# Optimization experiments

Hardware: AMD Instinct MI355X
Metric: run time of the kernel (lower is better)

Reference implementation:

```python
import jax, jax.numpy as jnp
import numpy as np
import math

B, T, E = 16, 4096, 1024
WIN = 15
EPS = 1e-6
HALF = T // 2


def _make_linear(key, out_f, in_f):
    k1, k2 = jax.random.split(key)
    lim = 1.0 / math.sqrt(in_f)
    W = jax.random.uniform(k1, (out_f, in_f), minval=-lim, maxval=lim, dtype=jnp.float32)
    b = jax.random.uniform(k2, (out_f,), minval=-lim, maxval=lim, dtype=jnp.float32)
    return W, b


def setup_inputs() -> dict:
    key = jax.random.key(0)
    ks = jax.random.split(key, 5)
    x = jax.random.normal(ks[0], (B, T, E), dtype=jnp.float32)
    taper = jnp.linspace(1.0, 0.0, T, dtype=jnp.float32)
    cW1, cb1 = _make_linear(ks[1], HALF, T)
    cW2, cb2 = _make_linear(ks[2], HALF, HALF)
    pW1, pb1 = _make_linear(ks[3], HALF, T)
    pW2, pb2 = _make_linear(ks[4], HALF, HALF)
    return {"x": x, "taper": taper,
            "cW1": cW1, "cb1": cb1, "cW2": cW2, "cb2": cb2,
            "pW1": pW1, "pb1": pb1, "pW2": pW2, "pb2": pb2}


def _compressor(h, W1, b1, W2, b2):
    # Linear -> SiLU -> Linear -> Tanh  (torch Linear: y = h @ W^T + b)
    h = jax.nn.silu(h @ W1.T + b1)
    return jnp.tanh(h @ W2.T + b2)


def _tdiff_raw(c0):
    Bb, Tt = c0.shape
    xp = jnp.pad(c0, ((0, 0), (WIN, 0)))  # left pad with zeros
    num = jnp.zeros_like(c0)
    for d in range(1, WIN + 1):  # small fixed loop over window lags
        num = num + float(d) * jax.lax.dynamic_slice_in_dim(xp, WIN - d, Tt, axis=1)
    i = jnp.arange(Tt, dtype=jnp.float32)
    s = jnp.minimum(i, float(WIN))
    norm = s * (s + 1.0) * 0.5
    return jnp.where(norm > 0, num / jnp.maximum(norm, 1.0), 0.0)


def reference(x, taper, cW1, cb1, cW2, cb2, pW1, pb1, pW2, pb2):
    x_t = x * taper[None, :, None]          # (B,T,E) tapered in time
    c0 = x_t[..., 0]                         # (B,T)
    r = jnp.abs(c0) + EPS
    start = jnp.where(c0 >= 0, 0.0, jnp.float32(math.pi))
    v = jnp.clip(x_t[..., 1:] / r[..., None], -1.0 + EPS, 1.0 - EPS)
    phases = start + jnp.arcsin(v).sum(axis=-1)  # (B,T)
    tdiff = _compressor(_tdiff_raw(c0), pW1, pb1, pW2, pb2)   # (B,T/2)
    thash = _compressor(phases, cW1, cb1, cW2, cb2)           # (B,T/2)
    return jnp.stack([thash, tdiff], axis=-1)                 # (B,T/2,2)
```

## Files before the change

### kernel.cpp

```cpp
#include <hip/hip_runtime.h>
#include <math.h>

#define BB 16
#define TT 4096
#define EE 1024
#define HALF 2048
#define WIN 15
#define EPSF 1e-6f
#define PI_F   3.14159265358979323846f
#define PIO2_F 1.57079632679489662f

__device__ __forceinline__ float fast_asinf(float v) {
    float a  = fabsf(v);
    float z1 = a * a;
    float z2 = 0.5f * (1.0f - a);
    bool big = a > 0.5f;
    float z = big ? z2 : z1;
    float s = big ? sqrtf(z) : a;
    float p = fmaf(z, 4.2163199048e-2f, 2.4181311049e-2f);
    p = fmaf(z, p, 4.5470025998e-2f);
    p = fmaf(z, p, 7.4953002686e-2f);
    p = fmaf(z, p, 1.6666752422e-1f);
    float r = fmaf(s * z, p, s);
    float rb = fmaf(-2.0f, r, PIO2_F);
    r = big ? rb : r;
    return copysignf(r, v);
}

__global__ void phase_tdiff_kernel(const float* __restrict__ x,
                                   const float* __restrict__ taper,
                                   float* __restrict__ phases_b,
                                   float* __restrict__ tdiff_b) {
    const int wave = threadIdx.x >> 6;
    const int lane = threadIdx.x & 63;
    const int row  = blockIdx.x * 4 + wave;
    const int b = row >> 12;
    const int t = row & (TT - 1);
    const float tap = taper[t];
    const float* xr = x + (size_t)row * EE;

    float xd = 0.0f, tapd = 0.0f;
    const int td = t - lane;
    const bool do_d = (lane >= 1) && (lane <= WIN) && (lane <= t);
    if (do_d) {
        xd   = x[((size_t)b * TT + td) * EE];
        tapd = taper[td];
    }

    const float c0 = xr[0] * tap;
    const float r = fabsf(c0) + EPSF;
    const float scale = tap / r;
    const float start = (c0 >= 0.0f) ? 0.0f : PI_F;
    const float LO = -1.0f + EPSF, HI = 1.0f - EPSF;

    const float4* xr4 = (const float4*)xr;
    float sum = 0.0f;
    #pragma unroll
    for (int j = 0; j < 4; ++j) {
        float4 v = xr4[j * 64 + lane];
        float a0 = fast_asinf(fminf(fmaxf(v.x * scale, LO), HI));
        if ((j | lane) == 0) a0 = 0.0f;
        sum += a0;
        sum += fast_asinf(fminf(fmaxf(v.y * scale, LO), HI));
        sum += fast_asinf(fminf(fmaxf(v.z * scale, LO), HI));
        sum += fast_asinf(fminf(fmaxf(v.w * scale, LO), HI));
    }
    #pragma unroll
    for (int off = 32; off > 0; off >>= 1)
        sum += __shfl_xor(sum, off, 64);

    float contrib = do_d ? ((float)lane * xd * tapd) : 0.0f;
    #pragma unroll
    for (int off = 8; off > 0; off >>= 1)
        contrib += __shfl_xor(contrib, off, 64);

    if (lane == 0) {
        phases_b[b * TT + t] = start + sum;
        const int s = (t < WIN) ? t : WIN;
        const float norm = 0.5f * (float)s * (float)(s + 1);
        tdiff_b[b * TT + t] = (norm > 0.0f) ? (contrib / norm) : 0.0f;
    }
}

__device__ __forceinline__ void gld_lds16(const float* g, float* l) {
    __builtin_amdgcn_global_load_lds(
        (const __attribute__((address_space(1))) unsigned int*)g,
        (__attribute__((address_space(3))) unsigned int*)l,
        16, 0, 0);
}

template <int K, int MODE>
__global__ void __launch_bounds__(256)
gemm_kernel(const float* __restrict__ A0, const float* __restrict__ W0,
            const float* __restrict__ bias0, float* __restrict__ out0,
            const float* __restrict__ A1, const float* __restrict__ W1,
            const float* __restrict__ bias1, float* __restrict__ out1) {
    constexpr int KT = 512;
    constexpr int NT = K / KT;
    constexpr int LROW = KT + 4;
    __shared__ float als[2][16 * LROW];

    const int nb = HALF / 8;
    const int g = blockIdx.x / nb;
    const int obase = (blockIdx.x % nb) * 8;

    const float* A    = g ? A1 : A0;
    const float* W    = g ? W1 : W0;
    const float* bias = g ? bias1 : bias0;
    float* out        = g ? out1 : out0;

    const int wv   = threadIdx.x >> 6;
    const int lane = threadIdx.x & 63;
    const int col0 = obase + wv * 2;
    const int col1 = col0 + 1;
    const float* w0p = W + (size_t)col0 * K;
    const float* w1p = W + (size_t)col1 * K;

    auto stage = [&](int t, int s) {
        #pragma unroll
        for (int i = 0; i < 4; ++i) {
            const int br = wv * 4 + i;
            const float* src = A + (size_t)br * K + t * KT + lane * 4;
            float* dst = &als[s][br * LROW];
            gld_lds16(src, dst);
            gld_lds16(src + 256, dst + 256);
        }
    };

    float acc0[16], acc1[16];
    #pragma unroll
    for (int i = 0; i < 16; ++i) { acc0[i] = 0.0f; acc1[i] = 0.0f; }

    stage(0, 0);

    for (int t = 0; t < NT; ++t) {
        const int cur = t & 1;

        float4 w0v[2], w1v[2];
        #pragma unroll
        for (int s2 = 0; s2 < 2; ++s2) {
            w0v[s2] = *(const float4*)(w0p + t * KT + s2 * 256 + lane * 4);
            w1v[s2] = *(const float4*)(w1p + t * KT + s2 * 256 + lane * 4);
        }

        if (t + 1 < NT) {
            stage(t + 1, cur ^ 1);
            asm volatile("s_waitcnt vmcnt(8)" ::: "memory");
        } else {
            asm volatile("s_waitcnt vmcnt(0)" ::: "memory");
        }
        __builtin_amdgcn_s_barrier();
        __builtin_amdgcn_sched_barrier(0);

        #pragma unroll
        for (int s2 = 0; s2 < 2; ++s2) {
            #pragma unroll
            for (int br = 0; br < 16; ++br) {
                const float4 a4 = *(const float4*)&als[cur][br * LROW + s2 * 256 + lane * 4];
                acc0[br] += w0v[s2].x*a4.x + w0v[s2].y*a4.y + w0v[s2].z*a4.z + w0v[s2].w*a4.w;
                acc1[br] += w1v[s2].x*a4.x + w1v[s2].y*a4.y + w1v[s2].z*a4.z + w1v[s2].w*a4.w;
            }
        }
        __builtin_amdgcn_sched_barrier(0);
        __builtin_amdgcn_s_barrier();
    }

    #pragma unroll
    for (int off = 32; off > 0; off >>= 1) {
        #pragma unroll
        for (int i = 0; i < 16; ++i) {
            acc0[i] += __shfl_xor(acc0[i], off, 64);
            acc1[i] += __shfl_xor(acc1[i], off, 64);
        }
    }

    const bool isw0 = (lane == 0), isw1 = (lane == 32);
    if (isw0 || isw1) {
        const int o = isw0 ? col0 : col1;
        const float bs = bias[o];
        #pragma unroll
        for (int i = 0; i < 16; ++i) {
            float s = (isw0 ? acc0[i] : acc1[i]) + bs;
            if (MODE == 0) {
                s = s / (1.0f + expf(-s));
                out[(size_t)i * HALF + o] = s;
            } else {
                s = tanhf(s);
                out[(size_t)i * (HALF * 2) + o * 2 + g] = s;
            }
        }
    }
}

extern "C" void kernel_launch(void* const* d_in, const int* in_sizes, int n_in,
                              void* d_out, int out_size, void* d_ws, size_t ws_size,
                              hipStream_t stream) {
    const float* x     = (const float*)d_in[0];
    const float* taper = (const float*)d_in[1];
    const float* cW1   = (const float*)d_in[2];
    const float* cb1   = (const float*)d_in[3];
    const float* cW2   = (const float*)d_in[4];
    const float* cb2   = (const float*)d_in[5];
    const float* pW1   = (const float*)d_in[6];
    const float* pb1   = (const float*)d_in[7];
    const float* pW2   = (const float*)d_in[8];
    const float* pb2   = (const float*)d_in[9];
    float* out = (float*)d_out;
    float* ws  = (float*)d_ws;

    float* phases_b = ws;
    float* tdiff_b  = ws + 65536;
    float* H1_b     = ws + 131072;
    float* H2_b     = ws + 163840;

    phase_tdiff_kernel<<<BB * TT / 4, 256, 0, stream>>>(x, taper, phases_b, tdiff_b);
    gemm_kernel<TT, 0><<<512, 256, 0, stream>>>(phases_b, cW1, cb1, H1_b,
                                                tdiff_b, pW1, pb1, H2_b);
    gemm_kernel<HALF, 1><<<512, 256, 0, stream>>>(H1_b, cW2, cb2, out,
                                                  H2_b, pW2, pb2, out);
}
```

Measured before the change: 109.0 us.

## Deepen GEMM pipeline to four-stage ring with 512-thread blocks

Restructures the skinny GEMM kernels to use 8 waves per block covering 16 output columns, with a smaller K tile and a four-slot LDS ring. Both the activation tile (via global_load_lds) and the weight registers are prefetched three tiles ahead, with explicit vmcnt waits. The goal is to keep more weight-stream loads in flight and hide memory latency. In exchange it halves the grid to 256 blocks, raises register pressure from the four weight slots, and drops the LDS row padding, which may cause bank conflicts.

```diff
diff --git a/kernel.cpp b/kernel.cpp
--- a/kernel.cpp
+++ b/kernel.cpp
@@ -90,80 +90,86 @@
 }
 
 template <int K, int MODE>
-__global__ void __launch_bounds__(256)
+__global__ void __launch_bounds__(512)
 gemm_kernel(const float* __restrict__ A0, const float* __restrict__ W0,
             const float* __restrict__ bias0, float* __restrict__ out0,
             const float* __restrict__ A1, const float* __restrict__ W1,
             const float* __restrict__ bias1, float* __restrict__ out1) {
-    constexpr int KT = 512;
+    constexpr int KT = 256;
     constexpr int NT = K / KT;
-    constexpr int LROW = KT + 4;
-    __shared__ float als[2][16 * LROW];
-
-    const int nb = HALF / 8;
+    __shared__ float als[4][16][KT];
+
+    const int nb = HALF / 16;
     const int g = blockIdx.x / nb;
-    const int obase = (blockIdx.x % nb) * 8;
+    const int obase = (blockIdx.x % nb) * 16;
 
     const float* A    = g ? A1 : A0;
     const float* W    = g ? W1 : W0;
     const float* bias = g ? bias1 : bias0;
     float* out        = g ? out1 : out0;
 
-    const int wv   = threadIdx.x >> 6;
-    const int lane = threadIdx.x & 63;
+    const int wv    = threadIdx.x >> 6;
+    const int lane  = threadIdx.x & 63;
+    const int lane4 = lane * 4;
     const int col0 = obase + wv * 2;
     const int col1 = col0 + 1;
     const float* w0p = W + (size_t)col0 * K;
     const float* w1p = W + (size_t)col1 * K;
-
-    auto stage = [&](int t, int s) {
-        #pragma unroll
-        for (int i = 0; i < 4; ++i) {
-            const int br = wv * 4 + i;
-            const float* src = A + (size_t)br * K + t * KT + lane * 4;
-            float* dst = &als[s][br * LROW];
-            gld_lds16(src, dst);
-            gld_lds16(src + 256, dst + 256);
-        }
-    };
-
+    const int r0 = wv * 2, r1 = r0 + 1;
+
+    float4 wr0[4], wr1[4];
     float acc0[16], acc1[16];
     #pragma unroll
     for (int i = 0; i < 16; ++i) { acc0[i] = 0.0f; acc1[i] = 0.0f; }
 
-    stage(0, 0);
-
-    for (int t = 0; t < NT; ++t) {
-        const int cur = t & 1;
-
-        float4 w0v[2], w1v[2];
-        #pragma unroll
-        for (int s2 = 0; s2 < 2; ++s2) {
-            w0v[s2] = *(const float4*)(w0p + t * KT + s2 * 256 + lane * 4);
-            w1v[s2] = *(const float4*)(w1p + t * KT + s2 * 256 + lane * 4);
-        }
-
-        if (t + 1 < NT) {
-            stage(t + 1, cur ^ 1);
-            asm volatile("s_waitcnt vmcnt(8)" ::: "memory");
-        } else {
-            asm volatile("s_waitcnt vmcnt(0)" ::: "memory");
-        }
-        __builtin_amdgcn_s_barrier();
-        __builtin_amdgcn_sched_barrier(0);
-
-        #pragma unroll
-        for (int s2 = 0; s2 < 2; ++s2) {
-            #pragma unroll
-            for (int br = 0; br < 16; ++br) {
-                const float4 a4 = *(const float4*)&als[cur][br * LROW + s2 * 256 + lane * 4];
-                acc0[br] += w0v[s2].x*a4.x + w0v[s2].y*a4.y + w0v[s2].z*a4.z + w0v[s2].w*a4.w;
-                acc1[br] += w1v[s2].x*a4.x + w1v[s2].y*a4.y + w1v[s2].z*a4.z + w1v[s2].w*a4.w;
-            }
-        }
-        __builtin_amdgcn_sched_barrier(0);
-        __builtin_amdgcn_s_barrier();
-    }
+#define ISSUE_TILE(T, SL) do {                                            \
+        const int t_ = (T);                                               \
+        gld_lds16(A + (size_t)r0 * K + t_ * KT + lane4, &als[SL][r0][0]); \
+        gld_lds16(A + (size_t)r1 * K + t_ * KT + lane4, &als[SL][r1][0]); \
+        wr0[SL] = *(const float4*)(w0p + (size_t)t_ * KT + lane4);        \
+        wr1[SL] = *(const float4*)(w1p + (size_t)t_ * KT + lane4);        \
+    } while (0)
+
+#define COMPUTE_TILE(SL) do {                                             \
+        _Pragma("unroll")                                                 \
+        for (int br = 0; br < 16; ++br) {                                 \
+            const float4 a4 = *(const float4*)&als[SL][br][lane4];        \
+            acc0[br] += wr0[SL].x*a4.x + wr0[SL].y*a4.y                   \
+                      + wr0[SL].z*a4.z + wr0[SL].w*a4.w;                  \
+            acc1[br] += wr1[SL].x*a4.x + wr1[SL].y*a4.y                   \
+                      + wr1[SL].z*a4.z + wr1[SL].w*a4.w;                  \
+        }                                                                 \
+    } while (0)
+
+#define PHASE(S, DO_ISSUE, VMIMM) do {                                    \
+        if (DO_ISSUE) ISSUE_TILE(tcur + (S) + 3, ((S) + 3) & 3);          \
+        asm volatile("s_waitcnt vmcnt(" VMIMM ")" ::: "memory");          \
+        __builtin_amdgcn_sched_barrier(0);                                \
+        __builtin_amdgcn_s_barrier();                                     \
+        COMPUTE_TILE((S));                                                \
+        __builtin_amdgcn_sched_barrier(0);                                \
+        __builtin_amdgcn_s_barrier();                                     \
+    } while (0)
+
+    ISSUE_TILE(0, 0);
+    ISSUE_TILE(1, 1);
+    ISSUE_TILE(2, 2);
+
+    int tcur = 0;
+    for (; tcur + 7 < NT; tcur += 4) {
+        PHASE(0, true, "12");
+        PHASE(1, true, "12");
+        PHASE(2, true, "12");
+        PHASE(3, true, "12");
+    }
+    PHASE(0, true,  "12");
+    PHASE(1, false, "8");
+    PHASE(2, false, "4");
+    PHASE(3, false, "0");
+
+#undef PHASE
+#undef COMPUTE_TILE
+#undef ISSUE_TILE
 
     #pragma unroll
     for (int off = 32; off > 0; off >>= 1) {
@@ -214,8 +220,8 @@
     float* H2_b     = ws + 163840;
 
     phase_tdiff_kernel<<<BB * TT / 4, 256, 0, stream>>>(x, taper, phases_b, tdiff_b);
-    gemm_kernel<TT, 0><<<512, 256, 0, stream>>>(phases_b, cW1, cb1, H1_b,
+    gemm_kernel<TT, 0><<<256, 512, 0, stream>>>(phases_b, cW1, cb1, H1_b,
                                                 tdiff_b, pW1, pb1, H2_b);
-    gemm_kernel<HALF, 1><<<512, 256, 0, stream>>>(H1_b, cW2, cb2, out,
+    gemm_kernel<HALF, 1><<<256, 512, 0, stream>>>(H1_b, cW2, cb2, out,
                                                   H2_b, pW2, pb2, out);
 }
```

Result: slower. 139.3 us (+27.8%).

## Fuse both compressor GEMM launches into one kernel with a grid barrier

Applied to the files above, without the earlier changes.

Merges the two GEMM launches into a single persistent kernel. A global atomic counter acts as a grid-wide barrier between the first layer (SiLU) and the second layer (tanh), and the phase kernel resets that counter at its start. The aim is to remove one kernel launch and the inter-kernel gap. In exchange it depends on all 512 blocks being co-resident, or it will deadlock, and it adds atomic spin-wait overhead.

```diff
diff --git a/kernel.cpp b/kernel.cpp
--- a/kernel.cpp
+++ b/kernel.cpp
@@ -30,7 +30,10 @@
 __global__ void phase_tdiff_kernel(const float* __restrict__ x,
                                    const float* __restrict__ taper,
                                    float* __restrict__ phases_b,
-                                   float* __restrict__ tdiff_b) {
+                                   float* __restrict__ tdiff_b,
+                                   int* __restrict__ barrier_ctr) {
+    if (blockIdx.x == 0 && threadIdx.x == 0) *barrier_ctr = 0;
+
     const int wave = threadIdx.x >> 6;
     const int lane = threadIdx.x & 63;
     const int row  = blockIdx.x * 4 + wave;
@@ -89,16 +92,20 @@
         16, 0, 0);
 }
 
+#define KT_G 512
+#define LROW (KT_G + 4)
+
 template <int K, int MODE>
-__global__ void __launch_bounds__(256)
-gemm_kernel(const float* __restrict__ A0, const float* __restrict__ W0,
-            const float* __restrict__ bias0, float* __restrict__ out0,
-            const float* __restrict__ A1, const float* __restrict__ W1,
-            const float* __restrict__ bias1, float* __restrict__ out1) {
-    constexpr int KT = 512;
-    constexpr int NT = K / KT;
-    constexpr int LROW = KT + 4;
-    __shared__ float als[2][16 * LROW];
+__device__ __forceinline__ void gemm_stage(const float* __restrict__ A0,
+                                           const float* __restrict__ W0,
+                                           const float* __restrict__ bias0,
+                                           float* __restrict__ out0,
+                                           const float* __restrict__ A1,
+                                           const float* __restrict__ W1,
+                                           const float* __restrict__ bias1,
+                                           float* __restrict__ out1,
+                                           float (*als)[16 * LROW]) {
+    constexpr int NT = K / KT_G;
 
     const int nb = HALF / 8;
     const int g = blockIdx.x / nb;
@@ -120,7 +127,7 @@
         #pragma unroll
         for (int i = 0; i < 4; ++i) {
             const int br = wv * 4 + i;
-            const float* src = A + (size_t)br * K + t * KT + lane * 4;
+            const float* src = A + (size_t)br * K + t * KT_G + lane * 4;
             float* dst = &als[s][br * LROW];
             gld_lds16(src, dst);
             gld_lds16(src + 256, dst + 256);
@@ -139,8 +146,8 @@
         float4 w0v[2], w1v[2];
         #pragma unroll
         for (int s2 = 0; s2 < 2; ++s2) {
-            w0v[s2] = *(const float4*)(w0p + t * KT + s2 * 256 + lane * 4);
-            w1v[s2] = *(const float4*)(w1p + t * KT + s2 * 256 + lane * 4);
+            w0v[s2] = *(const float4*)(w0p + t * KT_G + s2 * 256 + lane * 4);
+            w1v[s2] = *(const float4*)(w1p + t * KT_G + s2 * 256 + lane * 4);
         }
 
         if (t + 1 < NT) {
@@ -190,6 +197,33 @@
             }
         }
     }
+}
+
+__global__ void __launch_bounds__(256)
+gemm_fused_kernel(const float* phases_b, const float* tdiff_b,
+                  const float* cW1, const float* cb1,
+                  const float* cW2, const float* cb2,
+                  const float* pW1, const float* pb1,
+                  const float* pW2, const float* pb2,
+                  float* H1_b, float* H2_b, float* out,
+                  int* barrier_ctr) {
+    __shared__ float als[2][16 * LROW];
+
+    gemm_stage<TT, 0>(phases_b, cW1, cb1, H1_b, tdiff_b, pW1, pb1, H2_b, als);
+
+    __threadfence();
+    __syncthreads();
+    if (threadIdx.x == 0) {
+        __hip_atomic_fetch_add(barrier_ctr, 1, __ATOMIC_ACQ_REL,
+                               __HIP_MEMORY_SCOPE_AGENT);
+        while (__hip_atomic_load(barrier_ctr, __ATOMIC_ACQUIRE,
+                                 __HIP_MEMORY_SCOPE_AGENT) < 512) {
+            __builtin_amdgcn_s_sleep(2);
+        }
+    }
+    __syncthreads();
+
+    gemm_stage<HALF, 1>(H1_b, cW2, cb2, out, H2_b, pW2, pb2, out, als);
 }
 
 extern "C" void kernel_launch(void* const* d_in, const int* in_sizes, int n_in,
@@ -212,10 +246,12 @@
     float* tdiff_b  = ws + 65536;
     float* H1_b     = ws + 131072;
     float* H2_b     = ws + 163840;
-
-    phase_tdiff_kernel<<<BB * TT / 4, 256, 0, stream>>>(x, taper, phases_b, tdiff_b);
-    gemm_kernel<TT, 0><<<512, 256, 0, stream>>>(phases_b, cW1, cb1, H1_b,
-                                                tdiff_b, pW1, pb1, H2_b);
-    gemm_kernel<HALF, 1><<<512, 256, 0, stream>>>(H1_b, cW2, cb2, out,
-                                                  H2_b, pW2, pb2, out);
-}
+    int*   barrier_ctr = (int*)(ws + 196608);
+
+    phase_tdiff_kernel<<<BB * TT / 4, 256, 0, stream>>>(x, taper, phases_b,
+                                                        tdiff_b, barrier_ctr);
+    gemm_fused_kernel<<<512, 256, 0, stream>>>(phases_b, tdiff_b,
+                                               cW1, cb1, cW2, cb2,
+                                               pW1, pb1, pW2, pb2,
+                                               H1_b, H2_b, out, barrier_ctr);
+}
```

After: 160.2 us. +47.0%, slower.

## Split GEMM K-dimension across waves, with 8 output columns per thread and DPP reduction

Applied to the files above, without the earlier changes.

The skinny GEMM kernel is reorganized so that each wave covers a 128-wide K slice for all 8 output columns of the block, where before each wave computed 2 columns over the full K. Each A value read from LDS is now reused across 8 columns instead of 2. The loop is unrolled by two with explicit A/W double buffering. Partial sums are reduced with DPP row rotates instead of shuffles, then finished through an LDS cross-wave reduction. The cost is 128 accumulator registers per thread, which may reduce occupancy or cause spills, plus an extra LDS reduction pass.

```diff
diff --git a/kernel.cpp b/kernel.cpp
--- a/kernel.cpp
+++ b/kernel.cpp
@@ -89,6 +89,12 @@
         16, 0, 0);
 }
 
+template <int CTRL>
+__device__ __forceinline__ float dpp_ror_add(float v) {
+    int r = __builtin_amdgcn_update_dpp(0, __float_as_int(v), CTRL, 0xF, 0xF, false);
+    return v + __int_as_float(r);
+}
+
 template <int K, int MODE>
 __global__ void __launch_bounds__(256)
 gemm_kernel(const float* __restrict__ A0, const float* __restrict__ W0,
@@ -97,8 +103,9 @@
             const float* __restrict__ bias1, float* __restrict__ out1) {
     constexpr int KT = 512;
     constexpr int NT = K / KT;
-    constexpr int LROW = KT + 4;
-    __shared__ float als[2][16 * LROW];
+    constexpr int LR = KT + 4;
+    __shared__ float als[2][16 * LR];
+    float* redls = &als[0][0];
 
     const int nb = HALF / 8;
     const int g = blockIdx.x / nb;
@@ -111,85 +118,119 @@
 
     const int wv   = threadIdx.x >> 6;
     const int lane = threadIdx.x & 63;
-    const int col0 = obase + wv * 2;
-    const int col1 = col0 + 1;
-    const float* w0p = W + (size_t)col0 * K;
-    const float* w1p = W + (size_t)col1 * K;
-
-    auto stage = [&](int t, int s) {
+    const int kofs = wv * 128 + lane * 2;
+
+    const float* wb = W + (size_t)obase * K + kofs;
+
+    auto stageA = [&](int t) {
+        const int s = t & 1;
         #pragma unroll
         for (int i = 0; i < 4; ++i) {
             const int br = wv * 4 + i;
             const float* src = A + (size_t)br * K + t * KT + lane * 4;
-            float* dst = &als[s][br * LROW];
+            float* dst = &als[s][br * LR];
             gld_lds16(src, dst);
             gld_lds16(src + 256, dst + 256);
         }
     };
 
-    float acc0[16], acc1[16];
-    #pragma unroll
-    for (int i = 0; i < 16; ++i) { acc0[i] = 0.0f; acc1[i] = 0.0f; }
-
-    stage(0, 0);
-
-    for (int t = 0; t < NT; ++t) {
-        const int cur = t & 1;
-
-        float4 w0v[2], w1v[2];
-        #pragma unroll
-        for (int s2 = 0; s2 < 2; ++s2) {
-            w0v[s2] = *(const float4*)(w0p + t * KT + s2 * 256 + lane * 4);
-            w1v[s2] = *(const float4*)(w1p + t * KT + s2 * 256 + lane * 4);
-        }
-
-        if (t + 1 < NT) {
-            stage(t + 1, cur ^ 1);
-            asm volatile("s_waitcnt vmcnt(8)" ::: "memory");
+#define LOADW(WREG, T) do {                                               \
+        _Pragma("unroll")                                                 \
+        for (int c = 0; c < 8; ++c)                                       \
+            WREG[c] = *(const float2*)(wb + (size_t)c * K + (T) * KT);    \
+    } while (0)
+
+#define COMPUTE(S, WREG) do {                                             \
+        _Pragma("unroll")                                                 \
+        for (int b = 0; b < 16; ++b) {                                    \
+            const float2 a2 = *(const float2*)&als[S][b * LR + kofs];     \
+            _Pragma("unroll")                                             \
+            for (int c = 0; c < 8; ++c)                                   \
+                acc[c][b] += WREG[c].x * a2.x + WREG[c].y * a2.y;         \
+        }                                                                 \
+    } while (0)
+
+    float acc[8][16];
+    #pragma unroll
+    for (int c = 0; c < 8; ++c)
+        #pragma unroll
+        for (int b = 0; b < 16; ++b) acc[c][b] = 0.0f;
+
+    float2 wA[8], wB[8];
+    stageA(0);
+    LOADW(wA, 0);
+
+    #pragma unroll 1
+    for (int t = 0; t < NT; t += 2) {
+        stageA(t + 1);
+        LOADW(wB, t + 1);
+        asm volatile("s_waitcnt vmcnt(16)" ::: "memory");
+        __builtin_amdgcn_s_barrier();
+        __builtin_amdgcn_sched_barrier(0);
+        COMPUTE(0, wA);
+        __builtin_amdgcn_sched_barrier(0);
+        __builtin_amdgcn_s_barrier();
+
+        if (t + 2 < NT) {
+            stageA(t + 2);
+            LOADW(wA, t + 2);
+            asm volatile("s_waitcnt vmcnt(16)" ::: "memory");
         } else {
             asm volatile("s_waitcnt vmcnt(0)" ::: "memory");
         }
         __builtin_amdgcn_s_barrier();
         __builtin_amdgcn_sched_barrier(0);
-
-        #pragma unroll
-        for (int s2 = 0; s2 < 2; ++s2) {
+        COMPUTE(1, wB);
+        __builtin_amdgcn_sched_barrier(0);
+        __builtin_amdgcn_s_barrier();
+    }
+
+    #pragma unroll
+    for (int c = 0; c < 8; ++c)
+        #pragma unroll
+        for (int b = 0; b < 16; ++b) acc[c][b] = dpp_ror_add<0x121>(acc[c][b]);
+    #pragma unroll
+    for (int c = 0; c < 8; ++c)
+        #pragma unroll
+        for (int b = 0; b < 16; ++b) acc[c][b] = dpp_ror_add<0x122>(acc[c][b]);
+    #pragma unroll
+    for (int c = 0; c < 8; ++c)
+        #pragma unroll
+        for (int b = 0; b < 16; ++b) acc[c][b] = dpp_ror_add<0x124>(acc[c][b]);
+    #pragma unroll
+    for (int c = 0; c < 8; ++c)
+        #pragma unroll
+        for (int b = 0; b < 16; ++b) acc[c][b] = dpp_ror_add<0x128>(acc[c][b]);
+
+    if ((lane & 15) == 0) {
+        float* rp = redls + (wv * 4 + (lane >> 4)) * 128;
+        #pragma unroll
+        for (int c = 0; c < 8; ++c)
             #pragma unroll
-            for (int br = 0; br < 16; ++br) {
-                const float4 a4 = *(const float4*)&als[cur][br * LROW + s2 * 256 + lane * 4];
-                acc0[br] += w0v[s2].x*a4.x + w0v[s2].y*a4.y + w0v[s2].z*a4.z + w0v[s2].w*a4.w;
-                acc1[br] += w1v[s2].x*a4.x + w1v[s2].y*a4.y + w1v[s2].z*a4.z + w1v[s2].w*a4.w;
-            }
+            for (int b = 0; b < 16; b += 2)
+                *(float2*)&rp[c * 16 + b] = make_float2(acc[c][b], acc[c][b + 1]);
+    }
+    __syncthreads();
+
+    if (threadIdx.x < 128) {
+        const int c = threadIdx.x >> 4;
+        const int b = threadIdx.x & 15;
+        float s = 0.0f;
+        #pragma unroll
+        for (int j = 0; j < 16; ++j) s += redls[j * 128 + c * 16 + b];
+        const int o = obase + c;
+        s += bias[o];
+        if (MODE == 0) {
+            s = s / (1.0f + expf(-s));
+            out[(size_t)b * HALF + o] = s;
+        } else {
+            s = tanhf(s);
+            out[(size_t)b * (HALF * 2) + o * 2 + g] = s;
         }
-        __builtin_amdgcn_sched_barrier(0);
-        __builtin_amdgcn_s_barrier();
-    }
-
-    #pragma unroll
-    for (int off = 32; off > 0; off >>= 1) {
-        #pragma unroll
-        for (int i = 0; i < 16; ++i) {
-            acc0[i] += __shfl_xor(acc0[i], off, 64);
-            acc1[i] += __shfl_xor(acc1[i], off, 64);
-        }
-    }
-
-    const bool isw0 = (lane == 0), isw1 = (lane == 32);
-    if (isw0 || isw1) {
-        const int o = isw0 ? col0 : col1;
-        const float bs = bias[o];
-        #pragma unroll
-        for (int i = 0; i < 16; ++i) {
-            float s = (isw0 ? acc0[i] : acc1[i]) + bs;
-            if (MODE == 0) {
-                s = s / (1.0f + expf(-s));
-                out[(size_t)i * HALF + o] = s;
-            } else {
-                s = tanhf(s);
-                out[(size_t)i * (HALF * 2) + o * 2 + g] = s;
-            }
-        }
-    }
+    }
+
+#undef LOADW
+#undef COMPUTE
 }
 
 extern "C" void kernel_launch(void* const* d_in, const int* in_sizes, int n_in,
```

Result: slower. 120.0 us (+10.1%).
